# Kernel optimization log

Measured on AMD Instinct MI355X. Metric: run time of the kernel, lower is better.

## Reference

```python
import jax, jax.numpy as jnp
import numpy as np

N_USERS = 200000
N_ITEMS = 300000
N_TAGS = 100000
N_ENTITIES = N_ITEMS + N_TAGS          # 400000
N_NODES = N_USERS + N_ENTITIES         # 600000
N_EDGES = 10_000_000
DIM = 64
N_HOPS = 3
BATCH = 4096
K_NEG = 4
DECAY = 1e-4
EMB_SCALE = 0.02   # keeps BPR scores in a well-conditioned range after 3 hops
VAL_SCALE = 0.1    # mimics normalized adjacency values


def setup_inputs() -> dict:
    key = jax.random.key(0)
    k1, k2, k3, k4, k5, k6, k7 = jax.random.split(key, 7)
    all_embed = jax.random.normal(k1, (N_NODES, DIM), dtype=jnp.float32) * EMB_SCALE
    edge_row = jax.random.randint(k2, (N_EDGES,), 0, N_NODES)
    edge_col = jax.random.randint(k3, (N_EDGES,), 0, N_NODES)
    edge_val = jax.random.uniform(k4, (N_EDGES,), dtype=jnp.float32) * VAL_SCALE
    user = jax.random.randint(k5, (BATCH,), 0, N_USERS)
    pos_item = jax.random.randint(k6, (BATCH,), 0, N_ITEMS)
    neg_item = jax.random.randint(k7, (BATCH, K_NEG), 0, N_ITEMS)
    return {
        "all_embed": all_embed,
        "edge_val": edge_val,
        "edge_row": edge_row,
        "edge_col": edge_col,
        "user": user,
        "pos_item": pos_item,
        "neg_item": neg_item,
    }


def _gcn(all_embed, edge_val, edge_row, edge_col):
    # n_hops x SpMM(graph, x) with running sum of layer outputs (GraphConv.forward,
    # dropout disabled => eval path).
    x = all_embed                                   # [N_NODES, DIM]
    acc = x
    for _ in range(N_HOPS):
        # sparse COO matmul: out[r] += val * x[c]
        msgs = edge_val[:, None] * x[edge_col]      # [N_EDGES, DIM]
        x = jax.ops.segment_sum(msgs, edge_row, num_segments=N_NODES)
        acc = acc + x
    return acc


def reference(all_embed, edge_val, edge_row, edge_col, user, pos_item, neg_item):
    agg = _gcn(all_embed, edge_val, edge_row, edge_col)
    user_gcn = agg[:N_USERS]
    entity_gcn = agg[N_USERS:]

    u_e = user_gcn[user]                            # [B, D]
    pos_e = entity_gcn[pos_item]                    # [B, D]
    neg_e = entity_gcn[neg_item]                    # [B, K, D]

    pos_scores = jnp.sum(u_e * pos_e, axis=1)                 # [B]
    neg_scores = jnp.sum(u_e[:, None, :] * neg_e, axis=2)     # [B, K]
    mf_loss = -jnp.mean(jax.nn.log_sigmoid(pos_scores - neg_scores.mean(axis=1)))

    # L2 regularizer on the raw (pre-GCN) embeddings, as in Recommender.forward
    user_emb = all_embed[:N_USERS]
    entity_emb = all_embed[N_USERS:]
    regularizer = (jnp.sum(user_emb[user] ** 2)
                   + jnp.sum(entity_emb[pos_item] ** 2)
                   + jnp.sum(entity_emb[neg_item.reshape(-1)] ** 2)) / 2.0
    emb_loss = DECAY * regularizer / BATCH

    return (mf_loss + emb_loss, mf_loss, emb_loss)
```

## Files before the change

### kernel.cpp

```cpp
#include <hip/hip_runtime.h>
#include <hip/hip_fp16.h>

#define NU     200000
#define NNODES 600000
#define NE     10000000
#define DIM    64
#define BATCH  4096
#define KNEG   4
#define NSLOTS (BATCH * (2 + KNEG))
#define BSHIFT 7
#define BROWS  128
#define NBUCK  ((NNODES + BROWS - 1) / BROWS)
#define NBLK   1024
#define EPB    9768
#define QSCALE 40950.0f

#if __has_builtin(__builtin_amdgcn_cvt_f32_fp8)
__device__ __forceinline__ float dec8(unsigned int b) {
  return __builtin_amdgcn_cvt_f32_fp8((int)b, 0);
}
template <int J>
__device__ __forceinline__ float dec8w(unsigned int w32) {
  return __builtin_amdgcn_cvt_f32_fp8((int)w32, J);
}
#define DEC_SCALE (1.0f / QSCALE)
__device__ __forceinline__ float dec8_true(unsigned int b) { return dec8(b); }
#else
__device__ __forceinline__ float dec8(unsigned int b) {
  unsigned short h = (unsigned short)(((b & 0x80u) << 8) | ((b & 0x7Fu) << 7));
  return __half2float(__ushort_as_half(h));
}
template <int J>
__device__ __forceinline__ float dec8w(unsigned int w32) {
  return dec8((w32 >> (8 * J)) & 0xFFu);
}
#define DEC_SCALE (256.0f / QSCALE)
__device__ __forceinline__ float dec8_true(unsigned int b) {
  return dec8(b) * 256.0f;
}
#endif

__device__ __forceinline__ unsigned char enc8(float f) {
#if __has_builtin(__builtin_amdgcn_cvt_pk_fp8_f32)
  int r = __builtin_amdgcn_cvt_pk_fp8_f32(f, 0.0f, 0, false);
  return (unsigned char)(r & 0xFF);
#else
  unsigned int u = __float_as_uint(f);
  unsigned int s = (u >> 24) & 0x80u;
  float a = fabsf(f) * 0.00390625f;
  unsigned short h = __half_as_ushort(__float2half(a));
  unsigned int code = ((unsigned int)h + 0x3Fu + ((h >> 7) & 1u)) >> 7;
  if (code > 0x7Eu) code = 0x7Eu;
  return (unsigned char)(s | code);
#endif
}

__global__ __launch_bounds__(256) void conv_kernel(
    const float* __restrict__ in, unsigned char* __restrict__ out) {
  size_t i = ((size_t)blockIdx.x * 256 + threadIdx.x) * 4;
  if (i >= (size_t)NNODES * DIM) return;
  float4 v = *reinterpret_cast<const float4*>(in + i);
  uchar4 o;
  o.x = enc8(v.x); o.y = enc8(v.y); o.z = enc8(v.z); o.w = enc8(v.w);
  *reinterpret_cast<uchar4*>(out + i) = o;
}

__global__ __launch_bounds__(512) void hist2_kernel(const int* __restrict__ row,
                                                    int* __restrict__ cntT) {
  __shared__ int cnt[NBUCK];
  int b = blockIdx.x;
  int tid = threadIdx.x;
  for (int k = tid; k < NBUCK; k += 512) cnt[k] = 0;
  __syncthreads();
  int start = b * EPB;
  int lim = start + EPB;
  if (lim > NE) lim = NE;
  for (int base = start + tid * 4; base + 4 <= lim; base += 2048) {
    int4 r = *reinterpret_cast<const int4*>(row + base);
    atomicAdd(&cnt[r.x >> BSHIFT], 1);
    atomicAdd(&cnt[r.y >> BSHIFT], 1);
    atomicAdd(&cnt[r.z >> BSHIFT], 1);
    atomicAdd(&cnt[r.w >> BSHIFT], 1);
  }
  __syncthreads();
  int sb = ((b & 7) << 7) + (b >> 3);
  for (int k = tid; k < NBUCK; k += 512)
    cntT[(size_t)k * NBLK + sb] = cnt[k];
}

__global__ __launch_bounds__(256) void bktscan_kernel(int* __restrict__ cntT,
                                                      int* __restrict__ btot) {
  int k = (blockIdx.x * 256 + threadIdx.x) >> 6;
  if (k >= NBUCK) return;
  int lane = threadIdx.x & 63;
  int* r = cntT + (size_t)k * NBLK + lane * 16;
  int v[16];
#pragma unroll
  for (int j = 0; j < 4; ++j) {
    int4 a = reinterpret_cast<int4*>(r)[j];
    v[j * 4 + 0] = a.x; v[j * 4 + 1] = a.y;
    v[j * 4 + 2] = a.z; v[j * 4 + 3] = a.w;
  }
  int s = 0;
#pragma unroll
  for (int j = 0; j < 16; ++j) s += v[j];
  int inc = s;
  for (int off = 1; off < 64; off <<= 1) {
    int t = __shfl_up(inc, off);
    if (lane >= off) inc += t;
  }
  if (lane == 63) btot[k] = inc;
  int run = inc - s;
#pragma unroll
  for (int j = 0; j < 16; ++j) {
    int t = v[j];
    v[j] = run;
    run += t;
  }
#pragma unroll
  for (int j = 0; j < 4; ++j) {
    int4 a;
    a.x = v[j * 4 + 0]; a.y = v[j * 4 + 1];
    a.z = v[j * 4 + 2]; a.w = v[j * 4 + 3];
    reinterpret_cast<int4*>(r)[j] = a;
  }
}

__global__ __launch_bounds__(1024) void btotscan_kernel(
    const int* __restrict__ btot, int* __restrict__ bktbase) {
  __shared__ int lds[1024];
  int tid = threadIdx.x;
  int c[5];
  int s = 0;
#pragma unroll
  for (int j = 0; j < 5; ++j) {
    int b = tid * 5 + j;
    c[j] = (b < NBUCK) ? btot[b] : 0;
    s += c[j];
  }
  lds[tid] = s;
  __syncthreads();
  for (int off = 1; off < 1024; off <<= 1) {
    int v = (tid >= off) ? lds[tid - off] : 0;
    __syncthreads();
    lds[tid] += v;
    __syncthreads();
  }
  int run = lds[tid] - s;
#pragma unroll
  for (int j = 0; j < 5; ++j) {
    int b = tid * 5 + j;
    if (b < NBUCK) { bktbase[b] = run; run += c[j]; }
  }
  if (tid == 0) bktbase[NBUCK] = NE;
}

__global__ __launch_bounds__(512) void place_kernel(
    const int* __restrict__ row, const int* __restrict__ col,
    const float* __restrict__ val, const int* __restrict__ cntT,
    const int* __restrict__ bktbase, int2* __restrict__ binned) {
  __shared__ int cur[NBUCK];
  int b = blockIdx.x;
  int tid = threadIdx.x;
  int sb = ((b & 7) << 7) + (b >> 3);
  for (int k = tid; k < NBUCK; k += 512)
    cur[k] = bktbase[k] + cntT[(size_t)k * NBLK + sb];
  __syncthreads();
  int start = b * EPB;
  int lim = start + EPB;
  if (lim > NE) lim = NE;
  for (int base = start + tid * 4; base + 4 <= lim; base += 2048) {
    int4 r = *reinterpret_cast<const int4*>(row + base);
    int4 c = *reinterpret_cast<const int4*>(col + base);
    float4 v = *reinterpret_cast<const float4*>(val + base);
    int p;
    p = atomicAdd(&cur[r.x >> BSHIFT], 1);
    binned[p] = make_int2(c.x | ((r.x & (BROWS - 1)) << 20),
                          (int)(v.x * QSCALE + 0.5f));
    p = atomicAdd(&cur[r.y >> BSHIFT], 1);
    binned[p] = make_int2(c.y | ((r.y & (BROWS - 1)) << 20),
                          (int)(v.y * QSCALE + 0.5f));
    p = atomicAdd(&cur[r.z >> BSHIFT], 1);
    binned[p] = make_int2(c.z | ((r.z & (BROWS - 1)) << 20),
                          (int)(v.z * QSCALE + 0.5f));
    p = atomicAdd(&cur[r.w >> BSHIFT], 1);
    binned[p] = make_int2(c.w | ((r.w & (BROWS - 1)) << 20),
                          (int)(v.w * QSCALE + 0.5f));
  }
}

__global__ __launch_bounds__(512) void binB_kernel(
    const int2* __restrict__ binned, const int* __restrict__ bktbase,
    int* __restrict__ rowptr, int* __restrict__ ev) {
  __shared__ int cnt[BROWS], pref[BROWS], cur[BROWS];
  int b = blockIdx.x;
  int tid = threadIdx.x;
  int beg = bktbase[b], end = bktbase[b + 1];
  if (tid < BROWS) cnt[tid] = 0;
  __syncthreads();
  for (int i = beg + tid; i < end; i += 512)
    atomicAdd(&cnt[(binned[i].x >> 20) & (BROWS - 1)], 1);
  __syncthreads();
  if (tid < BROWS) pref[tid] = cnt[tid];
  __syncthreads();
  for (int off = 1; off < BROWS; off <<= 1) {
    int v = (tid < BROWS && tid >= off) ? pref[tid - off] : 0;
    __syncthreads();
    if (tid < BROWS) pref[tid] += v;
    __syncthreads();
  }
  if (tid < BROWS) {
    int begr = beg + pref[tid] - cnt[tid];
    cur[tid] = begr;
    rowptr[(b << BSHIFT) + tid] = begr;
  }
  __syncthreads();
  for (int i = beg + tid; i < end; i += 512) {
    int2 t = binned[i];
    int p = atomicAdd(&cur[(t.x >> 20) & (BROWS - 1)], 1);
    ev[p] = (t.x & 0xFFFFF) | (t.y << 20);
  }
}

__global__ __launch_bounds__(256) void mark_kernel(
    const int* __restrict__ user, const int* __restrict__ pos,
    const int* __restrict__ neg, const int* __restrict__ rowptr,
    const int* __restrict__ ev, unsigned char* __restrict__ flag) {
  int s = blockIdx.x * 256 + threadIdx.x;
  if (s >= NSLOTS) return;
  int node;
  if (s < BATCH) node = user[s];
  else if (s < 2 * BATCH) node = NU + pos[s - BATCH];
  else node = NU + neg[s - 2 * BATCH];
  flag[node] = 1;
  int beg = rowptr[node], end = rowptr[node + 1];
  for (int i = beg; i < end; ++i) flag[ev[i] & 0xFFFFF] = 1;
}

#define PROC1(e, idx)                                                        \
  {                                                                          \
    bool ok = ((idx) >= beg) && ((idx) < end);                               \
    int c = ok ? ((e) & 0xFFFFF) : 0;                                        \
    float qv = ok ? (float)((unsigned int)(e) >> 20) : 0.f;                  \
    unsigned int xw = *reinterpret_cast<const unsigned int*>(                \
        x + ((size_t)c << 6) + (q << 2));                                    \
    a0 = fmaf(qv, dec8w<0>(xw), a0);                                         \
    a1 = fmaf(qv, dec8w<1>(xw), a1);                                         \
    a2 = fmaf(qv, dec8w<2>(xw), a2);                                         \
    a3 = fmaf(qv, dec8w<3>(xw), a3);                                         \
  }

#define PROC4(E)                                                             \
  {                                                                          \
    PROC1((E).x, i + 0);                                                     \
    PROC1((E).y, i + 1);                                                     \
    PROC1((E).z, i + 2);                                                     \
    PROC1((E).w, i + 3);                                                     \
  }

template <bool USE_FLAG>
__global__ __launch_bounds__(256) void spmm_pull_kernel(
    const unsigned char* __restrict__ x, unsigned char* __restrict__ y,
    const int* __restrict__ ev, const int* __restrict__ rowptr,
    const unsigned char* __restrict__ flag) {
  int w = (blockIdx.x * 256 + threadIdx.x) >> 6;
  int lane = threadIdx.x & 63;
  int g = lane >> 4;
  int q = lane & 15;
  int row = (w << 2) + g;
  if (row >= NNODES) return;
  bool live = true;
  if (USE_FLAG) live = (flag[row] != 0);
  int beg = rowptr[row];
  int end = live ? rowptr[row + 1] : beg;
  float a0 = 0.f, a1 = 0.f, a2 = 0.f, a3 = 0.f;
  int i = beg & ~3;
  if (i < end) {
    int4 cur = *reinterpret_cast<const int4*>(ev + i);
    for (; i + 4 < end; i += 4) {
      int4 nxt = *reinterpret_cast<const int4*>(ev + i + 4);
      PROC4(cur);
      cur = nxt;
    }
    PROC4(cur);
  }
  if (live) {
    uchar4 o;
    o.x = enc8(a0 * DEC_SCALE); o.y = enc8(a1 * DEC_SCALE);
    o.z = enc8(a2 * DEC_SCALE); o.w = enc8(a3 * DEC_SCALE);
    *reinterpret_cast<uchar4*>(y + ((size_t)row << 6) + (q << 2)) = o;
  }
}

__global__ __launch_bounds__(256) void slot_pull_kernel(
    const unsigned char* __restrict__ x,
    float* __restrict__ accU, float* __restrict__ accP, float* __restrict__ accN,
    const int* __restrict__ user, const int* __restrict__ pos,
    const int* __restrict__ neg,
    const int* __restrict__ ev, const int* __restrict__ rowptr) {
  int w = (blockIdx.x * 256 + threadIdx.x) >> 6;
  int lane = threadIdx.x & 63;
  int g = lane >> 4;
  int q = lane & 15;
  int slot = (w << 2) + g;
  if (slot >= NSLOTS) return;
  int node;
  float* dst;
  if (slot < BATCH) {
    node = user[slot];
    dst = accU + (size_t)slot * DIM;
  } else if (slot < 2 * BATCH) {
    int b = slot - BATCH;
    node = NU + pos[b];
    dst = accP + (size_t)b * DIM;
  } else {
    int j = slot - 2 * BATCH;
    node = NU + neg[j];
    dst = accN + (size_t)j * DIM;
  }
  int beg = rowptr[node], end = rowptr[node + 1];
  float a0 = 0.f, a1 = 0.f, a2 = 0.f, a3 = 0.f;
  int i = beg & ~3;
  if (i < end) {
    int4 cur = *reinterpret_cast<const int4*>(ev + i);
    for (; i + 4 < end; i += 4) {
      int4 nxt = *reinterpret_cast<const int4*>(ev + i + 4);
      PROC4(cur);
      cur = nxt;
    }
    PROC4(cur);
  }
  float4* d = reinterpret_cast<float4*>(dst + (q << 2));
  float4 cv = *d;
  cv.x += a0 * DEC_SCALE; cv.y += a1 * DEC_SCALE;
  cv.z += a2 * DEC_SCALE; cv.w += a3 * DEC_SCALE;
  *d = cv;
}

__global__ __launch_bounds__(256) void gather_acc_f32(
    const float* __restrict__ x,
    float* __restrict__ accU, float* __restrict__ accP, float* __restrict__ accN,
    const int* __restrict__ user, const int* __restrict__ pos,
    const int* __restrict__ neg) {
  int t = blockIdx.x * 256 + threadIdx.x;
  int slot = t >> 4;
  if (slot >= NSLOTS) return;
  int sub = (t & 15) << 2;
  int node;
  float* dst;
  if (slot < BATCH) {
    node = user[slot];
    dst = accU + (size_t)slot * DIM;
  } else if (slot < 2 * BATCH) {
    int b = slot - BATCH;
    node = NU + pos[b];
    dst = accP + (size_t)b * DIM;
  } else {
    int j = slot - 2 * BATCH;
    node = NU + neg[j];
    dst = accN + (size_t)j * DIM;
  }
  float4 s = *reinterpret_cast<const float4*>(x + (size_t)node * DIM + sub);
  float4* d = reinterpret_cast<float4*>(dst + sub);
  float4 c = *d;
  c.x += s.x; c.y += s.y; c.z += s.z; c.w += s.w;
  *d = c;
}

__global__ __launch_bounds__(256) void gather_acc_fp8(
    const unsigned char* __restrict__ x,
    float* __restrict__ accU, float* __restrict__ accP, float* __restrict__ accN,
    const int* __restrict__ user, const int* __restrict__ pos,
    const int* __restrict__ neg) {
  int t = blockIdx.x * 256 + threadIdx.x;
  int slot = t >> 4;
  if (slot >= NSLOTS) return;
  int sub = (t & 15) << 2;
  int node;
  float* dst;
  if (slot < BATCH) {
    node = user[slot];
    dst = accU + (size_t)slot * DIM;
  } else if (slot < 2 * BATCH) {
    int b = slot - BATCH;
    node = NU + pos[b];
    dst = accP + (size_t)b * DIM;
  } else {
    int j = slot - 2 * BATCH;
    node = NU + neg[j];
    dst = accN + (size_t)j * DIM;
  }
  unsigned int s = *reinterpret_cast<const unsigned int*>(
      x + ((size_t)node << 6) + sub);
  float4* d = reinterpret_cast<float4*>(dst + sub);
  float4 c = *d;
  c.x += dec8w<0>(s) * (DEC_SCALE * QSCALE);
  c.y += dec8w<1>(s) * (DEC_SCALE * QSCALE);
  c.z += dec8w<2>(s) * (DEC_SCALE * QSCALE);
  c.w += dec8w<3>(s) * (DEC_SCALE * QSCALE);
  *d = c;
}

__global__ __launch_bounds__(256) void loss_kernel(
    const float* __restrict__ accU, const float* __restrict__ accP,
    const float* __restrict__ accN, const float* __restrict__ all_embed,
    const int* __restrict__ user, const int* __restrict__ pos,
    const int* __restrict__ neg, float* __restrict__ partial) {
  int gt = blockIdx.x * 256 + threadIdx.x;
  int b = gt >> 6;
  if (b >= BATCH) return;
  int lane = threadIdx.x & 63;

  float u = accU[(size_t)b * DIM + lane];
  float diff = u * accP[(size_t)b * DIM + lane];
  float nsum = 0.f;
  for (int k = 0; k < KNEG; ++k)
    nsum += u * accN[((size_t)b * KNEG + k) * DIM + lane];
  diff -= 0.25f * nsum;

  float ue = all_embed[(size_t)user[b] * DIM + lane];
  float pe = all_embed[(size_t)(NU + pos[b]) * DIM + lane];
  float reg = ue * ue + pe * pe;
  for (int k = 0; k < KNEG; ++k) {
    float ne = all_embed[(size_t)(NU + neg[b * KNEG + k]) * DIM + lane];
    reg += ne * ne;
  }

  for (int off = 1; off < 64; off <<= 1) {
    diff += __shfl_xor(diff, off);
    reg  += __shfl_xor(reg, off);
  }
  if (lane == 0) {
    float ls = (diff >= 0.f) ? -log1pf(expf(-diff))
                             : (diff - log1pf(expf(diff)));
    atomicAdd(partial + 0, -ls);
    atomicAdd(partial + 1, reg);
  }
}

__global__ void finalize_kernel(const float* __restrict__ partial,
                                float* __restrict__ out) {
  if (threadIdx.x == 0 && blockIdx.x == 0) {
    float mf  = partial[0] / (float)BATCH;
    float emb = 1e-4f * (partial[1] * 0.5f) / (float)BATCH;
    out[0] = mf + emb;
    out[1] = mf;
    out[2] = emb;
  }
}

extern "C" void kernel_launch(void* const* d_in, const int* in_sizes, int n_in,
                              void* d_out, int out_size, void* d_ws, size_t ws_size,
                              hipStream_t stream) {
  const float* all_embed = (const float*)d_in[0];
  const float* edge_val  = (const float*)d_in[1];
  const int*   edge_row  = (const int*)d_in[2];
  const int*   edge_col  = (const int*)d_in[3];
  const int*   user      = (const int*)d_in[4];
  const int*   pos       = (const int*)d_in[5];
  const int*   neg       = (const int*)d_in[6];
  float* out = (float*)d_out;

  char* base = (char*)d_ws;
  size_t off = 0;
  int2* binned = (int2*)(base + off);        off += (size_t)NE * 8;
  int* ev      = (int*)(base + off);         off += (size_t)NE * 4;
  int* rowptr  = (int*)(base + off);         off += (size_t)(NNODES + 192) * 4;
  int* cntT    = (int*)(base + off);         off += (size_t)NBUCK * NBLK * 4;
  int* btot    = (int*)(base + off);         off += (size_t)NBUCK * 4;
  int* bktbase = (int*)(base + off);         off += (size_t)(NBUCK + 1) * 4;
  off = (off + 255) & ~(size_t)255;
  unsigned char* flag = (unsigned char*)(base + off); off += NNODES;
  off = (off + 255) & ~(size_t)255;
  unsigned char* xq0   = (unsigned char*)(base + off); off += (size_t)NNODES * DIM;
  unsigned char* bufAq = (unsigned char*)(base + off); off += (size_t)NNODES * DIM;
  unsigned char* bufBq = (unsigned char*)(base + off); off += (size_t)NNODES * DIM;
  off = (off + 255) & ~(size_t)255;
  float* accU = (float*)(base + off);        off += (size_t)BATCH * DIM * 4;
  float* accP = (float*)(base + off);        off += (size_t)BATCH * DIM * 4;
  float* accN = (float*)(base + off);        off += (size_t)BATCH * KNEG * DIM * 4;
  float* partial = (float*)(base + off);

  size_t accBytes = ((size_t)BATCH * DIM * 2 + (size_t)BATCH * KNEG * DIM + 2) *
                    sizeof(float);

  int convBlocks = (int)(((size_t)NNODES * DIM / 4 + 255) / 256);
  int spBlocks   = NNODES / 16;
  int gaBlocks   = (NSLOTS * 16 + 255) / 256;
  int slBlocks   = NSLOTS / 16;
  int mkBlocks   = (NSLOTS + 255) / 256;
  int lsBlocks   = (BATCH * 64 + 255) / 256;

  hipMemsetAsync(flag, 0, NNODES, stream);
  hipMemsetAsync(accU, 0, accBytes, stream);

  conv_kernel<<<convBlocks, 256, 0, stream>>>(all_embed, xq0);
  hist2_kernel<<<NBLK, 512, 0, stream>>>(edge_row, cntT);
  bktscan_kernel<<<NBUCK / 4, 256, 0, stream>>>(cntT, btot);
  btotscan_kernel<<<1, 1024, 0, stream>>>(btot, bktbase);
  place_kernel<<<NBLK, 512, 0, stream>>>(edge_row, edge_col, edge_val,
                                         cntT, bktbase, binned);
  binB_kernel<<<NBUCK, 512, 0, stream>>>(binned, bktbase, rowptr, ev);
  mark_kernel<<<mkBlocks, 256, 0, stream>>>(user, pos, neg, rowptr, ev, flag);

  gather_acc_f32<<<gaBlocks, 256, 0, stream>>>(all_embed, accU, accP, accN,
                                               user, pos, neg);
  spmm_pull_kernel<false><<<spBlocks, 256, 0, stream>>>(xq0, bufAq, ev, rowptr,
                                                        flag);
  gather_acc_fp8<<<gaBlocks, 256, 0, stream>>>(bufAq, accU, accP, accN,
                                               user, pos, neg);
  spmm_pull_kernel<true><<<spBlocks, 256, 0, stream>>>(bufAq, bufBq, ev, rowptr,
                                                       flag);
  gather_acc_fp8<<<gaBlocks, 256, 0, stream>>>(bufBq, accU, accP, accN,
                                               user, pos, neg);
  slot_pull_kernel<<<slBlocks, 256, 0, stream>>>(bufBq, accU, accP, accN,
                                                 user, pos, neg, ev, rowptr);

  loss_kernel<<<lsBlocks, 256, 0, stream>>>(accU, accP, accN, all_embed,
                                            user, pos, neg, partial);
  finalize_kernel<<<1, 64, 0, stream>>>(partial, out);
}
```

Measured before the change: 725.7 us.

## Pad CSR rows to multiples of four via per-row counts and global scan

Per-row edge counts are now built with global atomics in the histogram kernel, then a three-kernel scan produces a row pointer where every row is padded to a multiple of four. Padding slots are zeroed ev entries (column 0, weight 0), so the SpMM inner loop reads aligned int4 chunks with no bounds masking or prefetch logic. The bin pass no longer needs its per-bucket count and scan, and fp8 decode now uses the packed two-at-a-time conversion. The trade-off is 10M global atomics, extra memsets of the padded edge array, and a few more small scan launches.

```diff
diff --git a/kernel.cpp b/kernel.cpp
--- a/kernel.cpp
+++ b/kernel.cpp
@@ -13,31 +13,39 @@
 #define NBUCK  ((NNODES + BROWS - 1) / BROWS)
 #define NBLK   1024
 #define EPB    9768
+#define EVCAP  (NE + 3 * NNODES)
+#define NBLK1R ((NNODES + 1023) / 1024)
 #define QSCALE 40950.0f
 
+typedef float f32x2 __attribute__((ext_vector_type(2)));
+
 #if __has_builtin(__builtin_amdgcn_cvt_f32_fp8)
-__device__ __forceinline__ float dec8(unsigned int b) {
-  return __builtin_amdgcn_cvt_f32_fp8((int)b, 0);
-}
 template <int J>
 __device__ __forceinline__ float dec8w(unsigned int w32) {
   return __builtin_amdgcn_cvt_f32_fp8((int)w32, J);
 }
 #define DEC_SCALE (1.0f / QSCALE)
-__device__ __forceinline__ float dec8_true(unsigned int b) { return dec8(b); }
+#define FP8_TRUE_SCALE 1.0f
 #else
-__device__ __forceinline__ float dec8(unsigned int b) {
+template <int J>
+__device__ __forceinline__ float dec8w(unsigned int w32) {
+  unsigned int b = (w32 >> (8 * J)) & 0xFFu;
   unsigned short h = (unsigned short)(((b & 0x80u) << 8) | ((b & 0x7Fu) << 7));
   return __half2float(__ushort_as_half(h));
 }
-template <int J>
-__device__ __forceinline__ float dec8w(unsigned int w32) {
-  return dec8((w32 >> (8 * J)) & 0xFFu);
-}
 #define DEC_SCALE (256.0f / QSCALE)
-__device__ __forceinline__ float dec8_true(unsigned int b) {
-  return dec8(b) * 256.0f;
-}
+#define FP8_TRUE_SCALE 256.0f
+#endif
+
+#if __has_builtin(__builtin_amdgcn_cvt_pk_f32_fp8)
+#define DEC4(xw)                                                  \
+  f32x2 lo = __builtin_amdgcn_cvt_pk_f32_fp8((int)(xw), false);   \
+  f32x2 hi = __builtin_amdgcn_cvt_pk_f32_fp8((int)(xw), true);    \
+  float d0 = lo.x, d1 = lo.y, d2 = hi.x, d3 = hi.y;
+#else
+#define DEC4(xw)                                                  \
+  float d0 = dec8w<0>(xw), d1 = dec8w<1>(xw),                     \
+        d2 = dec8w<2>(xw), d3 = dec8w<3>(xw);
 #endif
 
 __device__ __forceinline__ unsigned char enc8(float f) {
@@ -66,7 +74,8 @@
 }
 
 __global__ __launch_bounds__(512) void hist2_kernel(const int* __restrict__ row,
-                                                    int* __restrict__ cntT) {
+                                                    int* __restrict__ cntT,
+                                                    int* __restrict__ rowcnt) {
   __shared__ int cnt[NBUCK];
   int b = blockIdx.x;
   int tid = threadIdx.x;
@@ -81,11 +90,71 @@
     atomicAdd(&cnt[r.y >> BSHIFT], 1);
     atomicAdd(&cnt[r.z >> BSHIFT], 1);
     atomicAdd(&cnt[r.w >> BSHIFT], 1);
+    atomicAdd(&rowcnt[r.x], 1);
+    atomicAdd(&rowcnt[r.y], 1);
+    atomicAdd(&rowcnt[r.z], 1);
+    atomicAdd(&rowcnt[r.w], 1);
   }
   __syncthreads();
   int sb = ((b & 7) << 7) + (b >> 3);
   for (int k = tid; k < NBUCK; k += 512)
     cntT[(size_t)k * NBLK + sb] = cnt[k];
+}
+
+__device__ __forceinline__ int align4i(int x) { return (x + 3) & ~3; }
+
+__global__ __launch_bounds__(256) void rowscan1_kernel(
+    const int* __restrict__ in, int* __restrict__ out, int* __restrict__ bsum) {
+  __shared__ int lds[256];
+  int tid = threadIdx.x;
+  int base = blockIdx.x * 1024 + tid * 4;
+  int a[4];
+#pragma unroll
+  for (int j = 0; j < 4; ++j)
+    a[j] = (base + j < NNODES) ? align4i(in[base + j]) : 0;
+  int s = a[0] + a[1] + a[2] + a[3];
+  lds[tid] = s;
+  __syncthreads();
+  for (int off = 1; off < 256; off <<= 1) {
+    int v = (tid >= off) ? lds[tid - off] : 0;
+    __syncthreads();
+    lds[tid] += v;
+    __syncthreads();
+  }
+  int excl = lds[tid] - s;
+  if (tid == 255) bsum[blockIdx.x] = lds[255];
+  int run = excl;
+#pragma unroll
+  for (int j = 0; j < 4; ++j) {
+    if (base + j < NNODES) out[base + j] = run;
+    run += a[j];
+  }
+}
+
+__global__ __launch_bounds__(1024) void rowscan2_kernel(int* __restrict__ bsum,
+                                                        int n) {
+  __shared__ int lds[1024];
+  int tid = threadIdx.x;
+  int x = (tid < n) ? bsum[tid] : 0;
+  lds[tid] = x;
+  __syncthreads();
+  for (int off = 1; off < 1024; off <<= 1) {
+    int v = (tid >= off) ? lds[tid - off] : 0;
+    __syncthreads();
+    lds[tid] += v;
+    __syncthreads();
+  }
+  if (tid < n) bsum[tid] = lds[tid] - x;
+}
+
+__global__ __launch_bounds__(256) void rowscan3_kernel(
+    int* __restrict__ rowptr, const int* __restrict__ bsum,
+    const int* __restrict__ rowcnt) {
+  int i = blockIdx.x * 256 + threadIdx.x;
+  if (i >= NNODES) return;
+  int v = rowptr[i] + bsum[i >> 10];
+  rowptr[i] = v;
+  if (i == NNODES - 1) rowptr[NNODES] = v + align4i(rowcnt[i]);
 }
 
 __global__ __launch_bounds__(256) void bktscan_kernel(int* __restrict__ cntT,
@@ -126,45 +195,16 @@
   }
 }
 
-__global__ __launch_bounds__(1024) void btotscan_kernel(
-    const int* __restrict__ btot, int* __restrict__ bktbase) {
-  __shared__ int lds[1024];
-  int tid = threadIdx.x;
-  int c[5];
-  int s = 0;
-#pragma unroll
-  for (int j = 0; j < 5; ++j) {
-    int b = tid * 5 + j;
-    c[j] = (b < NBUCK) ? btot[b] : 0;
-    s += c[j];
-  }
-  lds[tid] = s;
-  __syncthreads();
-  for (int off = 1; off < 1024; off <<= 1) {
-    int v = (tid >= off) ? lds[tid - off] : 0;
-    __syncthreads();
-    lds[tid] += v;
-    __syncthreads();
-  }
-  int run = lds[tid] - s;
-#pragma unroll
-  for (int j = 0; j < 5; ++j) {
-    int b = tid * 5 + j;
-    if (b < NBUCK) { bktbase[b] = run; run += c[j]; }
-  }
-  if (tid == 0) bktbase[NBUCK] = NE;
-}
-
 __global__ __launch_bounds__(512) void place_kernel(
     const int* __restrict__ row, const int* __restrict__ col,
     const float* __restrict__ val, const int* __restrict__ cntT,
-    const int* __restrict__ bktbase, int2* __restrict__ binned) {
+    const int* __restrict__ rowptr, int2* __restrict__ binned) {
   __shared__ int cur[NBUCK];
   int b = blockIdx.x;
   int tid = threadIdx.x;
   int sb = ((b & 7) << 7) + (b >> 3);
   for (int k = tid; k < NBUCK; k += 512)
-    cur[k] = bktbase[k] + cntT[(size_t)k * NBLK + sb];
+    cur[k] = rowptr[k << BSHIFT] + cntT[(size_t)k * NBLK + sb];
   __syncthreads();
   int start = b * EPB;
   int lim = start + EPB;
@@ -190,30 +230,17 @@
 }
 
 __global__ __launch_bounds__(512) void binB_kernel(
-    const int2* __restrict__ binned, const int* __restrict__ bktbase,
-    int* __restrict__ rowptr, int* __restrict__ ev) {
-  __shared__ int cnt[BROWS], pref[BROWS], cur[BROWS];
+    const int2* __restrict__ binned, const int* __restrict__ rowptr,
+    const int* __restrict__ btot, int* __restrict__ ev) {
+  __shared__ int cur[BROWS];
   int b = blockIdx.x;
   int tid = threadIdx.x;
-  int beg = bktbase[b], end = bktbase[b + 1];
-  if (tid < BROWS) cnt[tid] = 0;
-  __syncthreads();
-  for (int i = beg + tid; i < end; i += 512)
-    atomicAdd(&cnt[(binned[i].x >> 20) & (BROWS - 1)], 1);
-  __syncthreads();
-  if (tid < BROWS) pref[tid] = cnt[tid];
-  __syncthreads();
-  for (int off = 1; off < BROWS; off <<= 1) {
-    int v = (tid < BROWS && tid >= off) ? pref[tid - off] : 0;
-    __syncthreads();
-    if (tid < BROWS) pref[tid] += v;
-    __syncthreads();
-  }
   if (tid < BROWS) {
-    int begr = beg + pref[tid] - cnt[tid];
-    cur[tid] = begr;
-    rowptr[(b << BSHIFT) + tid] = begr;
-  }
+    int rr = (b << BSHIFT) + tid;
+    cur[tid] = (rr < NNODES) ? rowptr[rr] : 0;
+  }
+  int beg = rowptr[b << BSHIFT];
+  int end = beg + btot[b];
   __syncthreads();
   for (int i = beg + tid; i < end; i += 512) {
     int2 t = binned[i];
@@ -237,25 +264,17 @@
   for (int i = beg; i < end; ++i) flag[ev[i] & 0xFFFFF] = 1;
 }
 
-#define PROC1(e, idx)                                                        \
+#define PROC1(e)                                                             \
   {                                                                          \
-    bool ok = ((idx) >= beg) && ((idx) < end);                               \
-    int c = ok ? ((e) & 0xFFFFF) : 0;                                        \
-    float qv = ok ? (float)((unsigned int)(e) >> 20) : 0.f;                  \
+    int c = (e) & 0xFFFFF;                                                   \
+    float qv = (float)((unsigned int)(e) >> 20);                             \
     unsigned int xw = *reinterpret_cast<const unsigned int*>(                \
-        x + ((size_t)c << 6) + (q << 2));                                    \
-    a0 = fmaf(qv, dec8w<0>(xw), a0);                                         \
-    a1 = fmaf(qv, dec8w<1>(xw), a1);                                         \
-    a2 = fmaf(qv, dec8w<2>(xw), a2);                                         \
-    a3 = fmaf(qv, dec8w<3>(xw), a3);                                         \
-  }
-
-#define PROC4(E)                                                             \
-  {                                                                          \
-    PROC1((E).x, i + 0);                                                     \
-    PROC1((E).y, i + 1);                                                     \
-    PROC1((E).z, i + 2);                                                     \
-    PROC1((E).w, i + 3);                                                     \
+        xq + ((size_t)c << 6));                                              \
+    DEC4(xw);                                                                \
+    a0 = fmaf(qv, d0, a0);                                                   \
+    a1 = fmaf(qv, d1, a1);                                                   \
+    a2 = fmaf(qv, d2, a2);                                                   \
+    a3 = fmaf(qv, d3, a3);                                                   \
   }
 
 template <bool USE_FLAG>
@@ -269,27 +288,18 @@
   int q = lane & 15;
   int row = (w << 2) + g;
   if (row >= NNODES) return;
-  bool live = true;
-  if (USE_FLAG) live = (flag[row] != 0);
-  int beg = rowptr[row];
-  int end = live ? rowptr[row + 1] : beg;
+  if (USE_FLAG && !flag[row]) return;
+  const unsigned char* xq = x + (q << 2);
+  int beg = rowptr[row], end = rowptr[row + 1];
   float a0 = 0.f, a1 = 0.f, a2 = 0.f, a3 = 0.f;
-  int i = beg & ~3;
-  if (i < end) {
-    int4 cur = *reinterpret_cast<const int4*>(ev + i);
-    for (; i + 4 < end; i += 4) {
-      int4 nxt = *reinterpret_cast<const int4*>(ev + i + 4);
-      PROC4(cur);
-      cur = nxt;
-    }
-    PROC4(cur);
-  }
-  if (live) {
-    uchar4 o;
-    o.x = enc8(a0 * DEC_SCALE); o.y = enc8(a1 * DEC_SCALE);
-    o.z = enc8(a2 * DEC_SCALE); o.w = enc8(a3 * DEC_SCALE);
-    *reinterpret_cast<uchar4*>(y + ((size_t)row << 6) + (q << 2)) = o;
-  }
+  for (int i = beg; i < end; i += 4) {
+    int4 e = *reinterpret_cast<const int4*>(ev + i);
+    PROC1(e.x); PROC1(e.y); PROC1(e.z); PROC1(e.w);
+  }
+  uchar4 o;
+  o.x = enc8(a0 * DEC_SCALE); o.y = enc8(a1 * DEC_SCALE);
+  o.z = enc8(a2 * DEC_SCALE); o.w = enc8(a3 * DEC_SCALE);
+  *reinterpret_cast<uchar4*>(y + ((size_t)row << 6) + (q << 2)) = o;
 }
 
 __global__ __launch_bounds__(256) void slot_pull_kernel(
@@ -318,17 +328,12 @@
     node = NU + neg[j];
     dst = accN + (size_t)j * DIM;
   }
+  const unsigned char* xq = x + (q << 2);
   int beg = rowptr[node], end = rowptr[node + 1];
   float a0 = 0.f, a1 = 0.f, a2 = 0.f, a3 = 0.f;
-  int i = beg & ~3;
-  if (i < end) {
-    int4 cur = *reinterpret_cast<const int4*>(ev + i);
-    for (; i + 4 < end; i += 4) {
-      int4 nxt = *reinterpret_cast<const int4*>(ev + i + 4);
-      PROC4(cur);
-      cur = nxt;
-    }
-    PROC4(cur);
+  for (int i = beg; i < end; i += 4) {
+    int4 e = *reinterpret_cast<const int4*>(ev + i);
+    PROC1(e.x); PROC1(e.y); PROC1(e.z); PROC1(e.w);
   }
   float4* d = reinterpret_cast<float4*>(dst + (q << 2));
   float4 cv = *d;
@@ -394,10 +399,11 @@
       x + ((size_t)node << 6) + sub);
   float4* d = reinterpret_cast<float4*>(dst + sub);
   float4 c = *d;
-  c.x += dec8w<0>(s) * (DEC_SCALE * QSCALE);
-  c.y += dec8w<1>(s) * (DEC_SCALE * QSCALE);
-  c.z += dec8w<2>(s) * (DEC_SCALE * QSCALE);
-  c.w += dec8w<3>(s) * (DEC_SCALE * QSCALE);
+  DEC4(s);
+  c.x += d0 * FP8_TRUE_SCALE;
+  c.y += d1 * FP8_TRUE_SCALE;
+  c.z += d2 * FP8_TRUE_SCALE;
+  c.w += d3 * FP8_TRUE_SCALE;
   *d = c;
 }
 
@@ -463,12 +469,13 @@
 
   char* base = (char*)d_ws;
   size_t off = 0;
-  int2* binned = (int2*)(base + off);        off += (size_t)NE * 8;
-  int* ev      = (int*)(base + off);         off += (size_t)NE * 4;
-  int* rowptr  = (int*)(base + off);         off += (size_t)(NNODES + 192) * 4;
+  int2* binned = (int2*)(base + off);        off += (size_t)EVCAP * 8;
+  int* ev      = (int*)(base + off);         off += (size_t)EVCAP * 4;
+  int* rowptr  = (int*)(base + off);         off += (size_t)(NNODES + 8) * 4;
+  int* rowcnt  = (int*)(base + off);         off += (size_t)NNODES * 4;
+  int* bsum    = (int*)(base + off);         off += 1024 * 4;
   int* cntT    = (int*)(base + off);         off += (size_t)NBUCK * NBLK * 4;
   int* btot    = (int*)(base + off);         off += (size_t)NBUCK * 4;
-  int* bktbase = (int*)(base + off);         off += (size_t)(NBUCK + 1) * 4;
   off = (off + 255) & ~(size_t)255;
   unsigned char* flag = (unsigned char*)(base + off); off += NNODES;
   off = (off + 255) & ~(size_t)255;
@@ -491,16 +498,21 @@
   int mkBlocks   = (NSLOTS + 255) / 256;
   int lsBlocks   = (BATCH * 64 + 255) / 256;
 
+  hipMemsetAsync(rowcnt, 0, (size_t)NNODES * 4, stream);
+  hipMemsetAsync(ev, 0, (size_t)EVCAP * 4, stream);
   hipMemsetAsync(flag, 0, NNODES, stream);
   hipMemsetAsync(accU, 0, accBytes, stream);
 
   conv_kernel<<<convBlocks, 256, 0, stream>>>(all_embed, xq0);
-  hist2_kernel<<<NBLK, 512, 0, stream>>>(edge_row, cntT);
+  hist2_kernel<<<NBLK, 512, 0, stream>>>(edge_row, cntT, rowcnt);
+  rowscan1_kernel<<<NBLK1R, 256, 0, stream>>>(rowcnt, rowptr, bsum);
+  rowscan2_kernel<<<1, 1024, 0, stream>>>(bsum, NBLK1R);
+  rowscan3_kernel<<<(NNODES + 255) / 256, 256, 0, stream>>>(rowptr, bsum,
+                                                            rowcnt);
   bktscan_kernel<<<NBUCK / 4, 256, 0, stream>>>(cntT, btot);
-  btotscan_kernel<<<1, 1024, 0, stream>>>(btot, bktbase);
   place_kernel<<<NBLK, 512, 0, stream>>>(edge_row, edge_col, edge_val,
-                                         cntT, bktbase, binned);
-  binB_kernel<<<NBUCK, 512, 0, stream>>>(binned, bktbase, rowptr, ev);
+                                         cntT, rowptr, binned);
+  binB_kernel<<<NBUCK, 512, 0, stream>>>(binned, rowptr, btot, ev);
   mark_kernel<<<mkBlocks, 256, 0, stream>>>(user, pos, neg, rowptr, ev, flag);
 
   gather_acc_f32<<<gaBlocks, 256, 0, stream>>>(all_embed, accU, accP, accN,
```

Measured after the change: 1.092 ms. 1.51x slower.
